# Optimization experiments

Hardware: AMD Instinct MI355X
Metric: run time of the kernel (lower is better)

The kernel has to match this reference:

```python
import jax, jax.numpy as jnp
import numpy as np

D_MODEL = 1024
N_HEADS = 16
D_K = D_MODEL // N_HEADS  # 64
SCALE = 1.0 / np.sqrt(D_K).astype(np.float32)


def setup_inputs() -> dict:
    key = jax.random.key(0)
    kx, kq, kk, kv, ko = jax.random.split(key, 5)
    B, S = 2, 2048
    s = 0.02  # keep pre-softmax logits in a sane range
    return {
        "x": jax.random.normal(kx, (B, S, D_MODEL), dtype=jnp.float32),
        "Wq": jax.random.normal(kq, (D_MODEL, D_MODEL), dtype=jnp.float32) * s,
        "Wk": jax.random.normal(kk, (D_MODEL, D_MODEL), dtype=jnp.float32) * s,
        "Wv": jax.random.normal(kv, (D_MODEL, D_MODEL), dtype=jnp.float32) * s,
        "Wo": jax.random.normal(ko, (D_MODEL, D_MODEL), dtype=jnp.float32) * s,
    }


def reference(x, Wq, Wk, Wv, Wo):
    # x: [B, S, D]; nn.Linear(bias=False) computes x @ W.T
    B, S, D = x.shape
    H, dk = N_HEADS, D_K

    def proj(W):
        # [B, S, D] -> [B, H, S, dk]
        return (x @ W.T).reshape(B, S, H, dk).transpose(0, 2, 1, 3)

    q = proj(Wq)
    k = proj(Wk)
    v = proj(Wv)

    # Flash tiling with online softmax is exact full attention (no mask):
    scores = jnp.einsum("bhqd,bhkd->bhqk", q, k) * SCALE  # [B,H,S,S]
    p = jax.nn.softmax(scores, axis=-1)
    o = jnp.einsum("bhqk,bhkd->bhqd", p, v)               # [B,H,S,dk]

    o = o.transpose(0, 2, 1, 3).reshape(B, S, D)
    return o @ Wo.T
```

## Files before the change

kernel.cpp:

```cpp
#include <hip/hip_runtime.h>
#include <cstdint>
#include <type_traits>

typedef __attribute__((ext_vector_type(8))) __bf16 bf16x8;
typedef __attribute__((ext_vector_type(4))) float f32x4;
typedef __attribute__((ext_vector_type(4))) short s16x4;
using u16 = unsigned short;
using u32 = unsigned int;

#define D_MODEL 1024
#define N_HEADS 16
#define D_K     64
#define SEQ     2048
#define BATCH   2
#define NTOKENS (BATCH * SEQ)
#define SCALE   0.125f
#define LOG2E   1.44269504088896340736f
#define C2      (SCALE * LOG2E)

__device__ __forceinline__ u16 f32_to_bf16(float f) {
    union { float f; u32 u; } v; v.f = f;
    u32 r = (v.u + 0x7fffu + ((v.u >> 16) & 1u)) >> 16;
    return (u16)r;
}

__device__ __forceinline__ u32 pack_bf16_pair(float a, float b) {
    u32 ua = __builtin_bit_cast(u32, a) + 0x8000u;
    u32 ub = __builtin_bit_cast(u32, b) + 0x8000u;
    return __builtin_amdgcn_perm(ub, ua, 0x07060302);
}

typedef const __attribute__((address_space(1))) u32* gas_ptr;
typedef __attribute__((address_space(3))) u32* las_ptr;
__device__ __forceinline__ void gl2lds16(const u16* g, u16* l) {
    __builtin_amdgcn_global_load_lds((gas_ptr)g, (las_ptr)l, 16, 0, 0);
}

__global__ __launch_bounds__(256) void cvt_bf16(const float* __restrict__ src,
                                                u16* __restrict__ dst, int n) {
    int i = (blockIdx.x * 256 + threadIdx.x) * 4;
    if (i < n) {
        float4 f = *(const float4*)(src + i);
        u32 lo = (u32)f32_to_bf16(f.x) | ((u32)f32_to_bf16(f.y) << 16);
        u32 hi = (u32)f32_to_bf16(f.z) | ((u32)f32_to_bf16(f.w) << 16);
        uint2 o; o.x = lo; o.y = hi;
        *(uint2*)(dst + i) = o;
    }
}

__global__ __launch_bounds__(256) void cvt_w4(const float* __restrict__ w0, const float* __restrict__ w1,
                                              const float* __restrict__ w2, const float* __restrict__ w3,
                                              u16* __restrict__ o0, u16* __restrict__ o1,
                                              u16* __restrict__ o2, u16* __restrict__ o3) {
    int k = blockIdx.y;
    const float* s = (k == 0) ? w0 : (k == 1) ? w1 : (k == 2) ? w2 : w3;
    u16*         d = (k == 0) ? o0 : (k == 1) ? o1 : (k == 2) ? o2 : o3;
    int i = (blockIdx.x * 256 + threadIdx.x) * 4;
    float4 f = *(const float4*)(s + i);
    u32 lo = (u32)f32_to_bf16(f.x) | ((u32)f32_to_bf16(f.y) << 16);
    u32 hi = (u32)f32_to_bf16(f.z) | ((u32)f32_to_bf16(f.w) << 16);
    uint2 o; o.x = lo; o.y = hi;
    *(uint2*)(d + i) = o;
}

__global__ __launch_bounds__(256) void gemm_qkv(const u16* __restrict__ xb,
                                                const u16* __restrict__ wq,
                                                const u16* __restrict__ wk,
                                                const u16* __restrict__ wv,
                                                u16* __restrict__ Qb, u16* __restrict__ Kb,
                                                u16* __restrict__ Vt) {
    __shared__ __align__(16) u16 As[128 * 32];
    __shared__ __align__(16) u16 Bs[128 * 32];

    const int tid  = threadIdx.x;
    const int wave = tid >> 6, lane = tid & 63;
    const int quad = lane >> 4, l4 = lane & 15;
    const int wm = wave >> 1, wn = wave & 1;
    const int bx = blockIdx.x, m0 = blockIdx.y * 128;
    const int kind = bx >> 3, nb = bx & 7;
    const u16* Bw = ((kind == 0) ? wq : (kind == 1) ? wk : wv) + (size_t)nb * 128 * D_MODEL;

    f32x4 acc[4][4] = {};

    const int r0 = wave * 16 + (lane >> 2);
    const int ch = (lane & 3) * 8;
    const u16* Ag0 = xb + (size_t)(m0 + r0) * D_MODEL + ch;
    const u16* Bg0 = Bw + (size_t)r0 * D_MODEL + ch;
    u16* AsW = As + wave * 512;
    u16* BsW = Bs + wave * 512;

    for (int kt = 0; kt < 32; ++kt) {
        const int ko = kt * 32;
        __syncthreads();
        gl2lds16(Ag0 + ko, AsW);
        gl2lds16(Ag0 + (size_t)64 * D_MODEL + ko, AsW + 2048);
        gl2lds16(Bg0 + ko, BsW);
        gl2lds16(Bg0 + (size_t)64 * D_MODEL + ko, BsW + 2048);
        __syncthreads();

        bf16x8 af[4], bfr[4];
#pragma unroll
        for (int mt = 0; mt < 4; mt++)
            af[mt] = *(const bf16x8*)&As[(wm * 64 + mt * 16 + l4) * 32 + quad * 8];
#pragma unroll
        for (int nt = 0; nt < 4; nt++)
            bfr[nt] = *(const bf16x8*)&Bs[(wn * 64 + nt * 16 + l4) * 32 + quad * 8];
#pragma unroll
        for (int mt = 0; mt < 4; mt++)
#pragma unroll
            for (int nt = 0; nt < 4; nt++)
                acc[mt][nt] = __builtin_amdgcn_mfma_f32_16x16x32_bf16(af[mt], bfr[nt], acc[mt][nt], 0, 0, 0);
    }

#pragma unroll
    for (int mt = 0; mt < 4; mt++)
#pragma unroll
        for (int nt = 0; nt < 4; nt++)
#pragma unroll
            for (int r = 0; r < 4; r++) {
                int m  = m0 + wm * 64 + mt * 16 + quad * 4 + r;
                int nl = nb * 128 + wn * 64 + nt * 16 + l4;
                float v = acc[mt][nt][r];
                if (kind == 0)      Qb[(size_t)m * D_MODEL + nl] = f32_to_bf16(v * C2);
                else if (kind == 1) Kb[(size_t)m * D_MODEL + nl] = f32_to_bf16(v);
                else                Vt[(size_t)nl * NTOKENS + m] = f32_to_bf16(v);
            }
}

__global__ __launch_bounds__(256) void gemm_out(const u16* __restrict__ A,
                                                const u16* __restrict__ Bw,
                                                float* __restrict__ C) {
    __shared__ __align__(16) u16 As[64 * 32];
    __shared__ __align__(16) u16 Bs[128 * 32];

    const int tid  = threadIdx.x;
    const int wave = tid >> 6, lane = tid & 63;
    const int quad = lane >> 4, l4 = lane & 15;
    const int m0 = blockIdx.y * 64, n0 = blockIdx.x * 128;

    f32x4 acc[4][2] = {};

    const int r0 = wave * 16 + (lane >> 2);
    const int ch = (lane & 3) * 8;
    const u16* Ag0 = A  + (size_t)(m0 + r0) * D_MODEL + ch;
    const u16* Bg0 = Bw + (size_t)(n0 + r0) * D_MODEL + ch;
    u16* AsW = As + wave * 512;
    u16* BsW = Bs + wave * 512;

    for (int kt = 0; kt < 32; ++kt) {
        const int ko = kt * 32;
        __syncthreads();
        gl2lds16(Ag0 + ko, AsW);
        gl2lds16(Bg0 + ko, BsW);
        gl2lds16(Bg0 + (size_t)64 * D_MODEL + ko, BsW + 2048);
        __syncthreads();

        bf16x8 af[4], bfr[2];
#pragma unroll
        for (int mt = 0; mt < 4; mt++)
            af[mt] = *(const bf16x8*)&As[(mt * 16 + l4) * 32 + quad * 8];
#pragma unroll
        for (int nt = 0; nt < 2; nt++)
            bfr[nt] = *(const bf16x8*)&Bs[(wave * 32 + nt * 16 + l4) * 32 + quad * 8];
#pragma unroll
        for (int mt = 0; mt < 4; mt++)
#pragma unroll
            for (int nt = 0; nt < 2; nt++)
                acc[mt][nt] = __builtin_amdgcn_mfma_f32_16x16x32_bf16(af[mt], bfr[nt], acc[mt][nt], 0, 0, 0);
    }

#pragma unroll
    for (int mt = 0; mt < 4; mt++)
#pragma unroll
        for (int nt = 0; nt < 2; nt++)
#pragma unroll
            for (int r = 0; r < 4; r++) {
                int m = m0 + mt * 16 + quad * 4 + r;
                int n = n0 + wave * 32 + nt * 16 + l4;
                C[(size_t)m * D_MODEL + n] = acc[mt][nt][r];
            }
}

__global__ __launch_bounds__(256) void attn(const u16* __restrict__ Q,
                                            const u16* __restrict__ K,
                                            const u16* __restrict__ Vt,
                                            u16* __restrict__ O) {
    __shared__ __align__(16) u16 Ks[2][64 * 72];
    __shared__ __align__(16) u16 Vs[2][64 * 72];

    const int tid  = threadIdx.x;
    const int wave = tid >> 6, lane = tid & 63;
    const int quad = lane >> 4, l4 = lane & 15;
    const int q0 = blockIdx.x * 128;
    const int h  = blockIdx.y;
    const int b  = blockIdx.z;
    const size_t headoff = (size_t)b * SEQ * D_MODEL + (size_t)h * D_K;

    const int sr = tid >> 2, sc = tid & 3;

    bf16x8 qa[2][2];
#pragma unroll
    for (int qs = 0; qs < 2; qs++) {
        const u16* qptr = Q + headoff + (size_t)(q0 + wave * 32 + qs * 16 + l4) * D_MODEL + quad * 8;
        qa[qs][0] = *(const bf16x8*)qptr;
        qa[qs][1] = *(const bf16x8*)(qptr + 32);
    }

    const u16* kbase = K + headoff;
    const u16* vbase = Vt + (size_t)(h * 64 + sr) * NTOKENS + (size_t)b * SEQ + sc * 16;

    int4 ka = *(const int4*)(kbase + (size_t)sr * D_MODEL + sc * 16);
    int4 kb = *(const int4*)(kbase + (size_t)sr * D_MODEL + sc * 16 + 8);
    int4 va = *(const int4*)(vbase);
    int4 vb = *(const int4*)(vbase + 8);

    f32x4 acc_o[2][4] = {};
    float lsum[2] = {0.f, 0.f};

    for (int it = 0; it < SEQ / 64; ++it) {
        u16* ks = Ks[it & 1];
        u16* vs = Vs[it & 1];
        *(int4*)&ks[sr * 72 + sc * 16]     = ka;
        *(int4*)&ks[sr * 72 + sc * 16 + 8] = kb;
        *(int4*)&vs[sr * 72 + sc * 16]     = va;
        *(int4*)&vs[sr * 72 + sc * 16 + 8] = vb;
        __syncthreads();

        const int kvn = ((it + 1) & 31) * 64;
        ka = *(const int4*)(kbase + (size_t)(kvn + sr) * D_MODEL + sc * 16);
        kb = *(const int4*)(kbase + (size_t)(kvn + sr) * D_MODEL + sc * 16 + 8);
        va = *(const int4*)(vbase + kvn);
        vb = *(const int4*)(vbase + kvn + 8);

        f32x4 sacc[2][4] = {};
#pragma unroll
        for (int nt = 0; nt < 4; nt++) {
            bf16x8 kb0 = *(const bf16x8*)&ks[(nt * 16 + l4) * 72 + quad * 8];
            bf16x8 kb1 = *(const bf16x8*)&ks[(nt * 16 + l4) * 72 + 32 + quad * 8];
#pragma unroll
            for (int qs = 0; qs < 2; qs++) {
                sacc[qs][nt] = __builtin_amdgcn_mfma_f32_16x16x32_bf16(kb0, qa[qs][0], sacc[qs][nt], 0, 0, 0);
                sacc[qs][nt] = __builtin_amdgcn_mfma_f32_16x16x32_bf16(kb1, qa[qs][1], sacc[qs][nt], 0, 0, 0);
            }
        }

        s16x4 pf[2][4];
#pragma unroll
        for (int qs = 0; qs < 2; qs++)
#pragma unroll
            for (int nt = 0; nt < 4; nt++) {
                float p0 = __builtin_amdgcn_exp2f(sacc[qs][nt][0]);
                float p1 = __builtin_amdgcn_exp2f(sacc[qs][nt][1]);
                float p2 = __builtin_amdgcn_exp2f(sacc[qs][nt][2]);
                float p3 = __builtin_amdgcn_exp2f(sacc[qs][nt][3]);
                lsum[qs] += (p0 + p1) + (p2 + p3);
                union { u32 u[2]; s16x4 v; } pp;
                pp.u[0] = pack_bf16_pair(p0, p1);
                pp.u[1] = pack_bf16_pair(p2, p3);
                pf[qs][nt] = pp.v;
            }

#pragma unroll
        for (int nt = 0; nt < 4; nt++)
#pragma unroll
            for (int dvt = 0; dvt < 4; dvt++) {
                s16x4 vfr = *(const s16x4*)&vs[(dvt * 16 + l4) * 72 + nt * 16 + quad * 4];
#pragma unroll
                for (int qs = 0; qs < 2; qs++)
                    acc_o[qs][dvt] = __builtin_amdgcn_mfma_f32_16x16x16bf16_1k(pf[qs][nt], vfr, acc_o[qs][dvt], 0, 0, 0);
            }
    }

#pragma unroll
    for (int qs = 0; qs < 2; qs++) {
        float ls = lsum[qs];
        ls += __shfl_xor(ls, 16, 64);
        ls += __shfl_xor(ls, 32, 64);
#pragma unroll
        for (int r = 0; r < 4; r++) {
            float linv = 1.f / __shfl(ls, quad * 4 + r, 64);
            int qrow = q0 + wave * 32 + qs * 16 + quad * 4 + r;
#pragma unroll
            for (int dvt = 0; dvt < 4; dvt++)
                O[headoff + (size_t)qrow * D_MODEL + dvt * 16 + l4] =
                    f32_to_bf16(acc_o[qs][dvt][r] * linv);
        }
    }
}

extern "C" void kernel_launch(void* const* d_in, const int* in_sizes, int n_in,
                              void* d_out, int out_size, void* d_ws, size_t ws_size,
                              hipStream_t stream) {
    const float* x  = (const float*)d_in[0];
    const float* Wq = (const float*)d_in[1];
    const float* Wk = (const float*)d_in[2];
    const float* Wv = (const float*)d_in[3];
    const float* Wo = (const float*)d_in[4];

    const int NX = NTOKENS * D_MODEL;
    const int NW = D_MODEL * D_MODEL;

    char* ws = (char*)d_ws;
    u16* xb = (u16*)ws;
    u16* wq = (u16*)(ws + (8u << 20));
    u16* wk = wq + NW;
    u16* wv = wk + NW;
    u16* wo = wv + NW;
    u16* Qb  = (u16*)(ws + (16u << 20));
    u16* Kb  = (u16*)(ws + (24u << 20));
    u16* Vtb = (u16*)(ws + (32u << 20));

    cvt_bf16<<<NX / 1024, 256, 0, stream>>>(x, xb, NX);
    cvt_w4<<<dim3(NW / 1024, 4), 256, 0, stream>>>(Wq, Wk, Wv, Wo, wq, wk, wv, wo);

    gemm_qkv<<<dim3(24, 32), 256, 0, stream>>>(xb, wq, wk, wv, Qb, Kb, Vtb);

    attn<<<dim3(SEQ / 128, N_HEADS, BATCH), 256, 0, stream>>>(Qb, Kb, Vtb, xb);

    gemm_out<<<dim3(8, 64), 256, 0, stream>>>(xb, wo, (float*)d_out);
}
```

Measured before the change: 199.5 us.

## Split attention KV range across wave pairs, merge conversions, compute V transposed

The attention kernel now handles 64 queries per block, with two wave pairs each covering half of the KV sequence. The halves are merged through LDS at the end, which doubles the grid and raises occupancy (launch bounds 3). The two fp32-to-bf16 conversion kernels are merged into one launch. The QKV GEMM now computes V as Wv·xᵀ so the transposed V stores are coalesced, and it is launched as a flat grid with m-fastest ordering. The cost is an extra reduction pass through LDS and two more syncs per block.

```diff
diff --git a/kernel.cpp b/kernel.cpp
--- a/kernel.cpp
+++ b/kernel.cpp
@@ -36,31 +36,28 @@
     __builtin_amdgcn_global_load_lds((gas_ptr)g, (las_ptr)l, 16, 0, 0);
 }
 
-__global__ __launch_bounds__(256) void cvt_bf16(const float* __restrict__ src,
-                                                u16* __restrict__ dst, int n) {
-    int i = (blockIdx.x * 256 + threadIdx.x) * 4;
-    if (i < n) {
-        float4 f = *(const float4*)(src + i);
-        u32 lo = (u32)f32_to_bf16(f.x) | ((u32)f32_to_bf16(f.y) << 16);
-        u32 hi = (u32)f32_to_bf16(f.z) | ((u32)f32_to_bf16(f.w) << 16);
-        uint2 o; o.x = lo; o.y = hi;
-        *(uint2*)(dst + i) = o;
-    }
-}
-
-__global__ __launch_bounds__(256) void cvt_w4(const float* __restrict__ w0, const float* __restrict__ w1,
-                                              const float* __restrict__ w2, const float* __restrict__ w3,
-                                              u16* __restrict__ o0, u16* __restrict__ o1,
-                                              u16* __restrict__ o2, u16* __restrict__ o3) {
-    int k = blockIdx.y;
-    const float* s = (k == 0) ? w0 : (k == 1) ? w1 : (k == 2) ? w2 : w3;
-    u16*         d = (k == 0) ? o0 : (k == 1) ? o1 : (k == 2) ? o2 : o3;
-    int i = (blockIdx.x * 256 + threadIdx.x) * 4;
-    float4 f = *(const float4*)(s + i);
+__global__ __launch_bounds__(256) void cvt_all(const float* __restrict__ x,
+                                               const float* __restrict__ Wq, const float* __restrict__ Wk,
+                                               const float* __restrict__ Wv, const float* __restrict__ Wo,
+                                               u16* __restrict__ xb,
+                                               u16* __restrict__ wq, u16* __restrict__ wk,
+                                               u16* __restrict__ wv, u16* __restrict__ wo) {
+    const int NX = NTOKENS * D_MODEL;
+    size_t i = (size_t)(blockIdx.x * 256 + threadIdx.x) * 4;
+    const float* src; u16* dst; size_t off;
+    if (i < (size_t)NX) { src = x; dst = xb; off = i; }
+    else {
+        size_t j = i - NX;
+        int w = (int)(j >> 20);
+        off = j & ((1u << 20) - 1);
+        src = (w == 0) ? Wq : (w == 1) ? Wk : (w == 2) ? Wv : Wo;
+        dst = (w == 0) ? wq : (w == 1) ? wk : (w == 2) ? wv : wo;
+    }
+    float4 f = *(const float4*)(src + off);
     u32 lo = (u32)f32_to_bf16(f.x) | ((u32)f32_to_bf16(f.y) << 16);
     u32 hi = (u32)f32_to_bf16(f.z) | ((u32)f32_to_bf16(f.w) << 16);
     uint2 o; o.x = lo; o.y = hi;
-    *(uint2*)(d + i) = o;
+    *(uint2*)(dst + off) = o;
 }
 
 __global__ __launch_bounds__(256) void gemm_qkv(const u16* __restrict__ xb,
@@ -76,16 +73,25 @@
     const int wave = tid >> 6, lane = tid & 63;
     const int quad = lane >> 4, l4 = lane & 15;
     const int wm = wave >> 1, wn = wave & 1;
-    const int bx = blockIdx.x, m0 = blockIdx.y * 128;
-    const int kind = bx >> 3, nb = bx & 7;
-    const u16* Bw = ((kind == 0) ? wq : (kind == 1) ? wk : wv) + (size_t)nb * 128 * D_MODEL;
+    const int f = blockIdx.x;
+
+    const u16 *Abase, *Bbase;
+    if (f < 512) {
+        const int m0 = (f & 31) * 128, t = f >> 5;
+        Abase = xb + (size_t)m0 * D_MODEL;
+        Bbase = ((t < 8) ? wq : wk) + (size_t)(t & 7) * 128 * D_MODEL;
+    } else {
+        const int g = f - 512;
+        Abase = wv + (size_t)(g & 7) * 128 * D_MODEL;
+        Bbase = xb + (size_t)(g >> 3) * 128 * D_MODEL;
+    }
 
     f32x4 acc[4][4] = {};
 
     const int r0 = wave * 16 + (lane >> 2);
     const int ch = (lane & 3) * 8;
-    const u16* Ag0 = xb + (size_t)(m0 + r0) * D_MODEL + ch;
-    const u16* Bg0 = Bw + (size_t)r0 * D_MODEL + ch;
+    const u16* Ag0 = Abase + (size_t)r0 * D_MODEL + ch;
+    const u16* Bg0 = Bbase + (size_t)r0 * D_MODEL + ch;
     u16* AsW = As + wave * 512;
     u16* BsW = Bs + wave * 512;
 
@@ -118,12 +124,19 @@
         for (int nt = 0; nt < 4; nt++)
 #pragma unroll
             for (int r = 0; r < 4; r++) {
-                int m  = m0 + wm * 64 + mt * 16 + quad * 4 + r;
-                int nl = nb * 128 + wn * 64 + nt * 16 + l4;
+                int mrow = wm * 64 + mt * 16 + quad * 4 + r;
+                int ncol = wn * 64 + nt * 16 + l4;
                 float v = acc[mt][nt][r];
-                if (kind == 0)      Qb[(size_t)m * D_MODEL + nl] = f32_to_bf16(v * C2);
-                else if (kind == 1) Kb[(size_t)m * D_MODEL + nl] = f32_to_bf16(v);
-                else                Vt[(size_t)nl * NTOKENS + m] = f32_to_bf16(v);
+                if (f < 512) {
+                    const int m0 = (f & 31) * 128, t = f >> 5;
+                    if (t < 8)
+                        Qb[(size_t)(m0 + mrow) * D_MODEL + (t & 7) * 128 + ncol] = f32_to_bf16(v * C2);
+                    else
+                        Kb[(size_t)(m0 + mrow) * D_MODEL + (t & 7) * 128 + ncol] = f32_to_bf16(v);
+                } else {
+                    const int g = f - 512;
+                    Vt[(size_t)((g & 7) * 128 + mrow) * NTOKENS + (g >> 3) * 128 + ncol] = f32_to_bf16(v);
+                }
             }
 }
 
@@ -181,110 +194,154 @@
             }
 }
 
-__global__ __launch_bounds__(256) void attn(const u16* __restrict__ Q,
-                                            const u16* __restrict__ K,
-                                            const u16* __restrict__ Vt,
-                                            u16* __restrict__ O) {
+__global__ __launch_bounds__(256, 3) void attn(const u16* __restrict__ Q,
+                                               const u16* __restrict__ K,
+                                               const u16* __restrict__ Vt,
+                                               u16* __restrict__ O) {
     __shared__ __align__(16) u16 Ks[2][64 * 72];
     __shared__ __align__(16) u16 Vs[2][64 * 72];
 
     const int tid  = threadIdx.x;
     const int wave = tid >> 6, lane = tid & 63;
     const int quad = lane >> 4, l4 = lane & 15;
-    const int q0 = blockIdx.x * 128;
+    const int pair = wave >> 1, w2 = wave & 1;
+    const int q0 = blockIdx.x * 64;
     const int h  = blockIdx.y;
     const int b  = blockIdx.z;
     const size_t headoff = (size_t)b * SEQ * D_MODEL + (size_t)h * D_K;
 
-    const int sr = tid >> 2, sc = tid & 3;
+    const int st = tid & 127, srow = st >> 1, shalf = st & 1;
+    const int kvp = pair * (SEQ / 2);
+
+    const u16* kptr = K + headoff + (size_t)(kvp + srow) * D_MODEL + shalf * 32;
+    const u16* vptr = Vt + (size_t)(h * 64 + srow) * NTOKENS + (size_t)b * SEQ + kvp + shalf * 32;
 
     bf16x8 qa[2][2];
 #pragma unroll
     for (int qs = 0; qs < 2; qs++) {
-        const u16* qptr = Q + headoff + (size_t)(q0 + wave * 32 + qs * 16 + l4) * D_MODEL + quad * 8;
-        qa[qs][0] = *(const bf16x8*)qptr;
-        qa[qs][1] = *(const bf16x8*)(qptr + 32);
-    }
-
-    const u16* kbase = K + headoff;
-    const u16* vbase = Vt + (size_t)(h * 64 + sr) * NTOKENS + (size_t)b * SEQ + sc * 16;
-
-    int4 ka = *(const int4*)(kbase + (size_t)sr * D_MODEL + sc * 16);
-    int4 kb = *(const int4*)(kbase + (size_t)sr * D_MODEL + sc * 16 + 8);
-    int4 va = *(const int4*)(vbase);
-    int4 vb = *(const int4*)(vbase + 8);
+        const u16* qp = Q + headoff + (size_t)(q0 + w2 * 32 + qs * 16 + l4) * D_MODEL + quad * 8;
+        qa[qs][0] = *(const bf16x8*)qp;
+        qa[qs][1] = *(const bf16x8*)(qp + 32);
+    }
+
+    int4 kr[4], vr[4];
+#pragma unroll
+    for (int j = 0; j < 4; j++) {
+        kr[j] = *(const int4*)(kptr + j * 8);
+        vr[j] = *(const int4*)(vptr + j * 8);
+    }
 
     f32x4 acc_o[2][4] = {};
     float lsum[2] = {0.f, 0.f};
 
-    for (int it = 0; it < SEQ / 64; ++it) {
-        u16* ks = Ks[it & 1];
-        u16* vs = Vs[it & 1];
-        *(int4*)&ks[sr * 72 + sc * 16]     = ka;
-        *(int4*)&ks[sr * 72 + sc * 16 + 8] = kb;
-        *(int4*)&vs[sr * 72 + sc * 16]     = va;
-        *(int4*)&vs[sr * 72 + sc * 16 + 8] = vb;
-        __syncthreads();
-
-        const int kvn = ((it + 1) & 31) * 64;
-        ka = *(const int4*)(kbase + (size_t)(kvn + sr) * D_MODEL + sc * 16);
-        kb = *(const int4*)(kbase + (size_t)(kvn + sr) * D_MODEL + sc * 16 + 8);
-        va = *(const int4*)(vbase + kvn);
-        vb = *(const int4*)(vbase + kvn + 8);
-
-        f32x4 sacc[2][4] = {};
-#pragma unroll
-        for (int nt = 0; nt < 4; nt++) {
-            bf16x8 kb0 = *(const bf16x8*)&ks[(nt * 16 + l4) * 72 + quad * 8];
-            bf16x8 kb1 = *(const bf16x8*)&ks[(nt * 16 + l4) * 72 + 32 + quad * 8];
-#pragma unroll
-            for (int qs = 0; qs < 2; qs++) {
-                sacc[qs][nt] = __builtin_amdgcn_mfma_f32_16x16x32_bf16(kb0, qa[qs][0], sacc[qs][nt], 0, 0, 0);
-                sacc[qs][nt] = __builtin_amdgcn_mfma_f32_16x16x32_bf16(kb1, qa[qs][1], sacc[qs][nt], 0, 0, 0);
-            }
-        }
-
-        s16x4 pf[2][4];
+    for (int it = 0; it < 16; ++it) {
+        u16* ksw = &Ks[pair][srow * 72 + shalf * 32];
+        u16* vsw = &Vs[pair][srow * 72 + shalf * 32];
+#pragma unroll
+        for (int j = 0; j < 4; j++) {
+            *(int4*)(ksw + j * 8) = kr[j];
+            *(int4*)(vsw + j * 8) = vr[j];
+        }
+        __syncthreads();
+
+        const int itn = (it + 1) & 15;
+#pragma unroll
+        for (int j = 0; j < 4; j++) {
+            kr[j] = *(const int4*)(kptr + (size_t)itn * 64 * D_MODEL + j * 8);
+            vr[j] = *(const int4*)(vptr + itn * 64 + j * 8);
+        }
+
+        const u16* ksr = Ks[pair];
+        const u16* vsr = Vs[pair];
+
+#pragma unroll
+        for (int half = 0; half < 2; half++) {
+            f32x4 sacc[2][2] = {};
+#pragma unroll
+            for (int n2 = 0; n2 < 2; n2++) {
+                const int nt = half * 2 + n2;
+                bf16x8 kb0 = *(const bf16x8*)&ksr[(nt * 16 + l4) * 72 + quad * 8];
+                bf16x8 kb1 = *(const bf16x8*)&ksr[(nt * 16 + l4) * 72 + 32 + quad * 8];
+#pragma unroll
+                for (int qs = 0; qs < 2; qs++) {
+                    sacc[qs][n2] = __builtin_amdgcn_mfma_f32_16x16x32_bf16(kb0, qa[qs][0], sacc[qs][n2], 0, 0, 0);
+                    sacc[qs][n2] = __builtin_amdgcn_mfma_f32_16x16x32_bf16(kb1, qa[qs][1], sacc[qs][n2], 0, 0, 0);
+                }
+            }
+            s16x4 pf[2][2];
+#pragma unroll
+            for (int qs = 0; qs < 2; qs++)
+#pragma unroll
+                for (int n2 = 0; n2 < 2; n2++) {
+                    float p0 = __builtin_amdgcn_exp2f(sacc[qs][n2][0]);
+                    float p1 = __builtin_amdgcn_exp2f(sacc[qs][n2][1]);
+                    float p2 = __builtin_amdgcn_exp2f(sacc[qs][n2][2]);
+                    float p3 = __builtin_amdgcn_exp2f(sacc[qs][n2][3]);
+                    lsum[qs] += (p0 + p1) + (p2 + p3);
+                    union { u32 u[2]; s16x4 v; } pp;
+                    pp.u[0] = pack_bf16_pair(p0, p1);
+                    pp.u[1] = pack_bf16_pair(p2, p3);
+                    pf[qs][n2] = pp.v;
+                }
+#pragma unroll
+            for (int n2 = 0; n2 < 2; n2++) {
+                const int nt = half * 2 + n2;
+#pragma unroll
+                for (int dvt = 0; dvt < 4; dvt++) {
+                    s16x4 vfr = *(const s16x4*)&vsr[(dvt * 16 + l4) * 72 + nt * 16 + quad * 4];
+#pragma unroll
+                    for (int qs = 0; qs < 2; qs++)
+                        acc_o[qs][dvt] = __builtin_amdgcn_mfma_f32_16x16x16bf16_1k(pf[qs][n2], vfr, acc_o[qs][dvt], 0, 0, 0);
+                }
+            }
+        }
+        __syncthreads();
+    }
+
+    float ls[2];
+#pragma unroll
+    for (int qs = 0; qs < 2; qs++) {
+        float t = lsum[qs];
+        t += __shfl_xor(t, 16, 64);
+        t += __shfl_xor(t, 32, 64);
+        ls[qs] = t;
+    }
+
+    float* Of = (float*)&Ks[0][0];
+    float* Lf = (float*)&Vs[0][0];
+    if (pair == 1) {
+#pragma unroll
+        for (int qs = 0; qs < 2; qs++) {
+#pragma unroll
+            for (int dvt = 0; dvt < 4; dvt++)
+#pragma unroll
+                for (int r = 0; r < 4; r++)
+                    Of[(w2 * 32 + qs * 16 + quad * 4 + r) * 64 + dvt * 16 + l4] = acc_o[qs][dvt][r];
+            if (quad == 0) Lf[w2 * 32 + qs * 16 + l4] = ls[qs];
+        }
+    }
+    __syncthreads();
+    if (pair == 0) {
+#pragma unroll
+        for (int qs = 0; qs < 2; qs++) {
+            ls[qs] += Lf[w2 * 32 + qs * 16 + l4];
+#pragma unroll
+            for (int dvt = 0; dvt < 4; dvt++)
+#pragma unroll
+                for (int r = 0; r < 4; r++)
+                    acc_o[qs][dvt][r] += Of[(w2 * 32 + qs * 16 + quad * 4 + r) * 64 + dvt * 16 + l4];
+        }
 #pragma unroll
         for (int qs = 0; qs < 2; qs++)
 #pragma unroll
-            for (int nt = 0; nt < 4; nt++) {
-                float p0 = __builtin_amdgcn_exp2f(sacc[qs][nt][0]);
-                float p1 = __builtin_amdgcn_exp2f(sacc[qs][nt][1]);
-                float p2 = __builtin_amdgcn_exp2f(sacc[qs][nt][2]);
-                float p3 = __builtin_amdgcn_exp2f(sacc[qs][nt][3]);
-                lsum[qs] += (p0 + p1) + (p2 + p3);
-                union { u32 u[2]; s16x4 v; } pp;
-                pp.u[0] = pack_bf16_pair(p0, p1);
-                pp.u[1] = pack_bf16_pair(p2, p3);
-                pf[qs][nt] = pp.v;
-            }
-
-#pragma unroll
-        for (int nt = 0; nt < 4; nt++)
-#pragma unroll
-            for (int dvt = 0; dvt < 4; dvt++) {
-                s16x4 vfr = *(const s16x4*)&vs[(dvt * 16 + l4) * 72 + nt * 16 + quad * 4];
-#pragma unroll
-                for (int qs = 0; qs < 2; qs++)
-                    acc_o[qs][dvt] = __builtin_amdgcn_mfma_f32_16x16x16bf16_1k(pf[qs][nt], vfr, acc_o[qs][dvt], 0, 0, 0);
-            }
-    }
-
-#pragma unroll
-    for (int qs = 0; qs < 2; qs++) {
-        float ls = lsum[qs];
-        ls += __shfl_xor(ls, 16, 64);
-        ls += __shfl_xor(ls, 32, 64);
-#pragma unroll
-        for (int r = 0; r < 4; r++) {
-            float linv = 1.f / __shfl(ls, quad * 4 + r, 64);
-            int qrow = q0 + wave * 32 + qs * 16 + quad * 4 + r;
-#pragma unroll
-            for (int dvt = 0; dvt < 4; dvt++)
-                O[headoff + (size_t)qrow * D_MODEL + dvt * 16 + l4] =
-                    f32_to_bf16(acc_o[qs][dvt][r] * linv);
-        }
+            for (int r = 0; r < 4; r++) {
+                float linv = 1.f / __shfl(ls[qs], quad * 4 + r, 64);
+                int qrow = q0 + w2 * 32 + qs * 16 + quad * 4 + r;
+#pragma unroll
+                for (int dvt = 0; dvt < 4; dvt++)
+                    O[headoff + (size_t)qrow * D_MODEL + dvt * 16 + l4] =
+                        f32_to_bf16(acc_o[qs][dvt][r] * linv);
+            }
     }
 }
 
@@ -297,7 +354,6 @@
     const float* Wv = (const float*)d_in[3];
     const float* Wo = (const float*)d_in[4];
 
-    const int NX = NTOKENS * D_MODEL;
     const int NW = D_MODEL * D_MODEL;
 
     char* ws = (char*)d_ws;
@@ -310,12 +366,11 @@
     u16* Kb  = (u16*)(ws + (24u << 20));
     u16* Vtb = (u16*)(ws + (32u << 20));
 
-    cvt_bf16<<<NX / 1024, 256, 0, stream>>>(x, xb, NX);
-    cvt_w4<<<dim3(NW / 1024, 4), 256, 0, stream>>>(Wq, Wk, Wv, Wo, wq, wk, wv, wo);
-
-    gemm_qkv<<<dim3(24, 32), 256, 0, stream>>>(xb, wq, wk, wv, Qb, Kb, Vtb);
-
-    attn<<<dim3(SEQ / 128, N_HEADS, BATCH), 256, 0, stream>>>(Qb, Kb, Vtb, xb);
+    cvt_all<<<8192, 256, 0, stream>>>(x, Wq, Wk, Wv, Wo, xb, wq, wk, wv, wo);
+
+    gemm_qkv<<<768, 256, 0, stream>>>(xb, wq, wk, wv, Qb, Kb, Vtb);
+
+    attn<<<dim3(SEQ / 64, N_HEADS, BATCH), 256, 0, stream>>>(Qb, Kb, Vtb, xb);
 
     gemm_out<<<dim3(8, 64), 256, 0, stream>>>(xb, wo, (float*)d_out);
 }
```

Result: slower. 365.3 us (+83.1%).
